# Kernel tuning notes

Hardware: AMD Instinct MI355X
Metric: run time of the kernel (lower is better)

The kernel has to match this reference:

```python
import jax, jax.numpy as jnp
import numpy as np

MARGIN = 0.5
BETA = 0.0
K = 5

def setup_inputs() -> dict:
    key = jax.random.key(0)
    k1, k2 = jax.random.split(key)
    n, d, n_classes = 4096, 512, 512
    inputs = jax.random.normal(k1, (n, d), dtype=jnp.float32)
    # L2-normalize as is standard for similarity-based DML embeddings
    inputs = inputs / jnp.linalg.norm(inputs, axis=1, keepdims=True)
    targets = jax.random.randint(k2, (n,), 0, n_classes, dtype=jnp.int64)
    return {"inputs": inputs, "targets": targets}

def reference(inputs, targets):
    n = inputs.shape[0]
    sim = inputs @ inputs.T                      # [n, n] similarity matrix
    same = targets[:, None] == targets[None, :]  # [n, n] same-class mask
    eye = jnp.eye(n, dtype=bool)
    pos_mask = same & ~eye                       # positive pairs (off-diagonal)
    neg_mask = ~same                             # negative pairs
    # margin_loss (hinge on similarity): pos -> [margin + beta - s]_+, neg -> [margin + s - beta]_+
    pos_l = jnp.maximum(MARGIN + BETA - sim, 0.0)
    neg_l = jnp.maximum(MARGIN + sim - BETA, 0.0)
    valid = pos_mask | neg_mask
    pair_loss = jnp.where(pos_mask, pos_l, neg_l)  # per-pair loss where valid
    num_of_zeros = jnp.sum(valid & (pair_loss == 0.0))
    # top-(4K) over the multiset of all valid pair losses (== topk of concat(pos_loss, neg_loss))
    masked = jnp.where(valid, pair_loss, -jnp.inf).reshape(-1)
    top_loss, _ = jax.lax.top_k(masked, 4 * K)
    loss = jnp.mean(top_loss)
    mean_pos_sim = jnp.sum(jnp.where(pos_mask, sim, 0.0)) / jnp.sum(pos_mask)
    mean_neg_sim = jnp.sum(jnp.where(neg_mask, sim, 0.0)) / jnp.sum(neg_mask)
    # NOTE: the original swaps the names: it returns mean(pos_sim) as `mean_neg_sim` and vice versa.
    return (loss, num_of_zeros, mean_pos_sim, mean_neg_sim)
```

## Files before the change

kernel.cpp:

```cpp
#include <hip/hip_runtime.h>
#include <hip/hip_fp16.h>

constexpr int N = 4096;
constexpr int D = 512;
constexpr int NT = 32;
constexpr int NBLK = NT * (NT + 1) / 2;
constexpr float SENT = -1e30f;
constexpr unsigned TCV = 8386560u;

constexpr float T0 = 0.60f;
constexpr unsigned CCAP = 320;

typedef _Float16 f16x8 __attribute__((ext_vector_type(8)));
typedef float f32x4 __attribute__((ext_vector_type(4)));

__device__ __forceinline__ void load_lds16(const _Float16* g, _Float16* l) {
  __builtin_amdgcn_global_load_lds(
      (const __attribute__((address_space(1))) void*)g,
      (__attribute__((address_space(3))) void*)l, 16, 0, 0);
}

template <int M>
__device__ __forceinline__ void wave_sel10(float (&vals)[M], float (&out)[10]) {
  int lane = threadIdx.x & 63;
  float lm = vals[0];
#pragma unroll
  for (int k = 1; k < M; k++) lm = fmaxf(lm, vals[k]);
#pragma unroll
  for (int r = 0; r < 10; r++) {
    float wmx = lm;
#pragma unroll
    for (int ofs = 1; ofs < 64; ofs <<= 1)
      wmx = fmaxf(wmx, __shfl_xor(wmx, ofs));
    out[r] = wmx;
    unsigned long long b = __ballot(lm == wmx);
    int leader = __ffsll(b) - 1;
    if (lane == leader) {
      bool found = false;
#pragma unroll
      for (int k = 0; k < M; k++) {
        bool hit = !found && (vals[k] == wmx);
        vals[k] = hit ? SENT : vals[k];
        found = found || hit;
      }
      lm = vals[0];
#pragma unroll
      for (int k = 1; k < M; k++) lm = fmaxf(lm, vals[k]);
    }
  }
}

constexpr int TOP10G_IDX = 1584;
constexpr int XH_OFF = 32768;

__global__ void prep_kernel(const float4* __restrict__ X4,
                            ushort4* __restrict__ Xh4) {
  int gid = blockIdx.x * 256 + threadIdx.x;
  float4 v = X4[gid];
  ushort4 o;
  o.x = __half_as_ushort(__float2half_rn(v.x));
  o.y = __half_as_ushort(__float2half_rn(v.y));
  o.z = __half_as_ushort(__float2half_rn(v.z));
  o.w = __half_as_ushort(__float2half_rn(v.w));
  Xh4[gid] = o;
}

__global__ __launch_bounds__(256, 3) void gemm_stats_kernel(
    const _Float16* __restrict__ Xh, const int* __restrict__ tgt,
    float* __restrict__ slots, float* __restrict__ top10g) {
  __shared__ _Float16 As[2][128 * 32];
  __shared__ _Float16 Bs[2][128 * 32];
  __shared__ int tA[128], tB[128];
  __shared__ float redf[2][4];
  __shared__ unsigned redu[4];
  __shared__ float wml[40];
  __shared__ float cbuf[CCAP];
  __shared__ unsigned ccnt;

  int tid = threadIdx.x;
  if (tid == 0) ccnt = 0u;

  int id = blockIdx.x, br = 0;
  while (id >= (NT - br)) { id -= (NT - br); br++; }
  int bc = br + id;

  if (tid < 128) tA[tid] = tgt[br * 128 + tid];
  else tB[tid - 128] = tgt[bc * 128 + (tid - 128)];

  int lane = tid & 63, wave = tid >> 6;
  int wm2 = (wave >> 1) << 6;
  int wn2 = (wave & 1) << 6;
  int lrow = lane & 15;
  int q4 = lane >> 4;
  int xk = (lrow >> 1) & 3;
  int quad4 = q4 * 4;

  int srow[2], scol[2], sdst[2];
#pragma unroll
  for (int i = 0; i < 2; i++) {
    int C = i * 256 + tid;
    int row = C >> 2, p = C & 3;
    srow[i] = row;
    scol[i] = (p ^ ((row >> 1) & 3)) * 8;
    sdst[i] = (i * 4 + wave) * 512;
  }
  const _Float16* Arow = Xh + (size_t)(br * 128) * D;
  const _Float16* Brow = Xh + (size_t)(bc * 128) * D;

#pragma unroll
  for (int i = 0; i < 2; i++) {
    load_lds16(Arow + srow[i] * D + scol[i], &As[0][sdst[i]]);
    load_lds16(Brow + srow[i] * D + scol[i], &Bs[0][sdst[i]]);
  }

  f32x4 acc[4][4] = {};
#pragma unroll
  for (int t = 0; t < 16; t++) {
    int cur = t & 1;
    __syncthreads();
    if (t < 15) {
      int k0 = (t + 1) * 32;
#pragma unroll
      for (int i = 0; i < 2; i++) {
        load_lds16(Arow + srow[i] * D + k0 + scol[i], &As[cur ^ 1][sdst[i]]);
        load_lds16(Brow + srow[i] * D + k0 + scol[i], &Bs[cur ^ 1][sdst[i]]);
      }
    }
    f16x8 af[4], bf[4];
#pragma unroll
    for (int mi = 0; mi < 4; mi++)
      af[mi] = *(const f16x8*)&As[cur][(wm2 + mi * 16 + lrow) * 32 +
                                       (q4 ^ xk) * 8];
#pragma unroll
    for (int ni = 0; ni < 4; ni++)
      bf[ni] = *(const f16x8*)&Bs[cur][(wn2 + ni * 16 + lrow) * 32 +
                                       (q4 ^ xk) * 8];
#pragma unroll
    for (int mi = 0; mi < 4; mi++)
#pragma unroll
      for (int ni = 0; ni < 4; ni++)
        acc[mi][ni] = __builtin_amdgcn_mfma_f32_16x16x32_f16(
            af[mi], bf[ni], acc[mi][ni], 0, 0, 0);
  }

  int tj[4];
#pragma unroll
  for (int ni = 0; ni < 4; ni++) tj[ni] = tB[wn2 + ni * 16 + lrow];

  float lsv = 0.f, lsp = 0.f;
  unsigned cz = 0;
  int ib = br * 128 + wm2 + quad4;
  int jb = bc * 128 + wn2 + lrow;
#pragma unroll
  for (int mi = 0; mi < 4; mi++) {
#pragma unroll
    for (int r = 0; r < 4; r++) {
      int trow = tA[wm2 + mi * 16 + quad4 + r];
      int i = ib + mi * 16 + r;
#pragma unroll
      for (int ni = 0; ni < 4; ni++) {
        float s = acc[mi][ni][r];
        int j = jb + ni * 16;
        bool valid = j > i;
        bool pos = valid && (trow == tj[ni]);
        float loss = fmaxf(0.5f + (pos ? -s : s), 0.0f);
        if (valid) {
          lsv += s;
          if (loss == 0.0f) cz += 0x10000u;
          if (loss >= T0) {
            unsigned p = atomicAdd(&ccnt, 1u);
            if (p < CCAP) cbuf[p] = loss;
          }
        }
        if (pos) { lsp += s; cz += 1u; }
      }
    }
  }
#pragma unroll
  for (int o = 32; o > 0; o >>= 1) {
    lsv += __shfl_down(lsv, o);
    lsp += __shfl_down(lsp, o);
    cz += __shfl_down(cz, o);
  }
  if (lane == 0) {
    redf[0][wave] = lsv; redf[1][wave] = lsp; redu[wave] = cz;
  }
  __syncthreads();

  if (tid == 192) {
    float a = 0.f, b = 0.f;
    unsigned c = 0;
#pragma unroll
    for (int w = 0; w < 4; w++) { a += redf[0][w]; b += redf[1][w]; c += redu[w]; }
    slots[blockIdx.x] = a;
    slots[NBLK + blockIdx.x] = b;
    ((unsigned*)slots)[2 * NBLK + blockIdx.x] = c;
  }

  unsigned cc = ccnt;
  if (cc >= 10u && cc <= CCAP) {
    if (wave == 0) {
      float m5[5];
#pragma unroll
      for (int k = 0; k < 5; k++) {
        unsigned g = lane + k * 64u;
        m5[k] = (g < cc) ? cbuf[g] : SENT;
      }
      float b10[10];
      wave_sel10<5>(m5, b10);
      if (lane == 0) {
#pragma unroll
        for (int r = 0; r < 10; r++) top10g[blockIdx.x * 10 + r] = b10[r];
      }
    }
  } else {
    float vals[64];
#pragma unroll
    for (int mi = 0; mi < 4; mi++) {
#pragma unroll
      for (int r = 0; r < 4; r++) {
        int trow = tA[wm2 + mi * 16 + quad4 + r];
        int i = ib + mi * 16 + r;
#pragma unroll
        for (int ni = 0; ni < 4; ni++) {
          float s = acc[mi][ni][r];
          int j = jb + ni * 16;
          bool valid = j > i;
          bool pos = valid && (trow == tj[ni]);
          float loss = fmaxf(0.5f + (pos ? -s : s), 0.0f);
          vals[(mi * 4 + ni) * 4 + r] = valid ? loss : SENT;
        }
      }
    }
    float wl[10];
    wave_sel10<64>(vals, wl);
    if (lane == 0) {
#pragma unroll
      for (int r = 0; r < 10; r++) wml[wave * 10 + r] = wl[r];
    }
    __syncthreads();
    if (wave == 0) {
      float m1[1];
      m1[0] = (lane < 40) ? wml[lane] : SENT;
      float b10[10];
      wave_sel10<1>(m1, b10);
      if (lane == 0) {
#pragma unroll
        for (int r = 0; r < 10; r++) top10g[blockIdx.x * 10 + r] = b10[r];
      }
    }
  }
}

__global__ __launch_bounds__(1024) void finalize_kernel(
    const float* __restrict__ slots, const float* __restrict__ top10g,
    float* __restrict__ out) {
  __shared__ float wml[160];
  __shared__ float redf[2][16];
  __shared__ unsigned redu[2][16];

  int tid = threadIdx.x, lane = tid & 63, wave = tid >> 6;

  float sv = 0.f, sp = 0.f;
  unsigned cv = 0, zz = 0;
  if (tid < NBLK) {
    sv = slots[tid];
    sp = slots[NBLK + tid];
    unsigned c = ((const unsigned*)slots)[2 * NBLK + tid];
    cv = c & 0xffffu;
    zz = c >> 16;
  }

  float v6[6];
#pragma unroll
  for (int k = 0; k < 6; k++) {
    int g = tid + k * 1024;
    v6[k] = (g < NBLK * 10) ? top10g[g] : SENT;
  }

#pragma unroll
  for (int o = 32; o > 0; o >>= 1) {
    sv += __shfl_down(sv, o);
    sp += __shfl_down(sp, o);
    cv += __shfl_down(cv, o);
    zz += __shfl_down(zz, o);
  }
  if (lane == 0) {
    redf[0][wave] = sv; redf[1][wave] = sp;
    redu[0][wave] = cv; redu[1][wave] = zz;
  }

  float wl[10];
  wave_sel10<6>(v6, wl);
  if (lane == 0) {
#pragma unroll
    for (int r = 0; r < 10; r++) wml[wave * 10 + r] = wl[r];
  }
  __syncthreads();

  if (wave == 0) {
    float m3[3];
#pragma unroll
    for (int k = 0; k < 3; k++) {
      int g = lane + k * 64;
      m3[k] = (g < 160) ? wml[g] : SENT;
    }
    float f10[10];
    wave_sel10<3>(m3, f10);
    if (lane == 0) {
      float topsum = 0.f;
#pragma unroll
      for (int r = 0; r < 10; r++) topsum += f10[r];
      float tsv = 0.f, tsp = 0.f;
      unsigned tcv = 0, tzz = 0;
#pragma unroll
      for (int w = 0; w < 16; w++) {
        tsv += redf[0][w]; tsp += redf[1][w];
        tcv += redu[0][w]; tzz += redu[1][w];
      }
      out[0] = topsum * 0.1f;
      out[1] = (float)(2u * tzz);
      out[2] = tsp / (float)tcv;
      out[3] = (tsv - tsp) / (float)(TCV - tcv);
    }
  }
}

extern "C" void kernel_launch(void* const* d_in, const int* in_sizes, int n_in,
                              void* d_out, int out_size, void* d_ws,
                              size_t ws_size, hipStream_t stream) {
  const float* X = (const float*)d_in[0];
  const int* tgt = (const int*)d_in[1];
  float* out = (float*)d_out;
  char* ws = (char*)d_ws;

  float* slots = (float*)ws;
  float* top10g = slots + TOP10G_IDX;
  _Float16* Xh = (_Float16*)(ws + XH_OFF);

  prep_kernel<<<(N * D / 4) / 256, 256, 0, stream>>>((const float4*)X,
                                                     (ushort4*)Xh);
  gemm_stats_kernel<<<NBLK, 256, 0, stream>>>(Xh, tgt, slots, top10g);
  finalize_kernel<<<1, 1024, 0, stream>>>(slots, top10g, out);
}
```

Measured before the change: 97.54 us.

## Triple-buffer GEMM loads, batch candidate atomics, binary-search fallback, prune finalize top-k

```diff
diff --git a/kernel.cpp b/kernel.cpp
--- a/kernel.cpp
+++ b/kernel.cpp
@@ -50,7 +50,8 @@
   }
 }
 
-constexpr int TOP10G_IDX = 1584;
+constexpr int BMAX_IDX = 3 * NBLK;
+constexpr int TOP10G_IDX = 4 * NBLK;
 constexpr int XH_OFF = 32768;
 
 __global__ void prep_kernel(const float4* __restrict__ X4,
@@ -68,14 +69,16 @@
 __global__ __launch_bounds__(256, 3) void gemm_stats_kernel(
     const _Float16* __restrict__ Xh, const int* __restrict__ tgt,
     float* __restrict__ slots, float* __restrict__ top10g) {
-  __shared__ _Float16 As[2][128 * 32];
-  __shared__ _Float16 Bs[2][128 * 32];
+  __shared__ _Float16 As[3][128 * 32];
+  __shared__ _Float16 Bs[3][128 * 32];
   __shared__ int tA[128], tB[128];
   __shared__ float redf[2][4];
   __shared__ unsigned redu[4];
-  __shared__ float wml[40];
+  __shared__ float redm[4];
+  __shared__ unsigned redc[4];
   __shared__ float cbuf[CCAP];
   __shared__ unsigned ccnt;
+  __shared__ unsigned scc;
 
   int tid = threadIdx.x;
   if (tid == 0) ccnt = 0u;
@@ -112,29 +115,40 @@
     load_lds16(Arow + srow[i] * D + scol[i], &As[0][sdst[i]]);
     load_lds16(Brow + srow[i] * D + scol[i], &Bs[0][sdst[i]]);
   }
+#pragma unroll
+  for (int i = 0; i < 2; i++) {
+    load_lds16(Arow + srow[i] * D + 32 + scol[i], &As[1][sdst[i]]);
+    load_lds16(Brow + srow[i] * D + 32 + scol[i], &Bs[1][sdst[i]]);
+  }
 
   f32x4 acc[4][4] = {};
 #pragma unroll
   for (int t = 0; t < 16; t++) {
-    int cur = t & 1;
-    __syncthreads();
     if (t < 15) {
-      int k0 = (t + 1) * 32;
+      asm volatile("s_waitcnt vmcnt(4) lgkmcnt(0)" ::: "memory");
+    } else {
+      asm volatile("s_waitcnt vmcnt(0) lgkmcnt(0)" ::: "memory");
+    }
+    __builtin_amdgcn_s_barrier();
+    if (t < 14) {
+      int k0 = (t + 2) * 32;
+      int nb = (t + 2) % 3;
 #pragma unroll
       for (int i = 0; i < 2; i++) {
-        load_lds16(Arow + srow[i] * D + k0 + scol[i], &As[cur ^ 1][sdst[i]]);
-        load_lds16(Brow + srow[i] * D + k0 + scol[i], &Bs[cur ^ 1][sdst[i]]);
-      }
-    }
+        load_lds16(Arow + srow[i] * D + k0 + scol[i], &As[nb][sdst[i]]);
+        load_lds16(Brow + srow[i] * D + k0 + scol[i], &Bs[nb][sdst[i]]);
+      }
+    }
+    int b = t % 3;
     f16x8 af[4], bf[4];
 #pragma unroll
     for (int mi = 0; mi < 4; mi++)
-      af[mi] = *(const f16x8*)&As[cur][(wm2 + mi * 16 + lrow) * 32 +
-                                       (q4 ^ xk) * 8];
+      af[mi] = *(const f16x8*)&As[b][(wm2 + mi * 16 + lrow) * 32 +
+                                     (q4 ^ xk) * 8];
 #pragma unroll
     for (int ni = 0; ni < 4; ni++)
-      bf[ni] = *(const f16x8*)&Bs[cur][(wn2 + ni * 16 + lrow) * 32 +
-                                       (q4 ^ xk) * 8];
+      bf[ni] = *(const f16x8*)&Bs[b][(wn2 + ni * 16 + lrow) * 32 +
+                                     (q4 ^ xk) * 8];
 #pragma unroll
     for (int mi = 0; mi < 4; mi++)
 #pragma unroll
@@ -146,75 +160,10 @@
   int tj[4];
 #pragma unroll
   for (int ni = 0; ni < 4; ni++) tj[ni] = tB[wn2 + ni * 16 + lrow];
-
-  float lsv = 0.f, lsp = 0.f;
-  unsigned cz = 0;
   int ib = br * 128 + wm2 + quad4;
   int jb = bc * 128 + wn2 + lrow;
-#pragma unroll
-  for (int mi = 0; mi < 4; mi++) {
-#pragma unroll
-    for (int r = 0; r < 4; r++) {
-      int trow = tA[wm2 + mi * 16 + quad4 + r];
-      int i = ib + mi * 16 + r;
-#pragma unroll
-      for (int ni = 0; ni < 4; ni++) {
-        float s = acc[mi][ni][r];
-        int j = jb + ni * 16;
-        bool valid = j > i;
-        bool pos = valid && (trow == tj[ni]);
-        float loss = fmaxf(0.5f + (pos ? -s : s), 0.0f);
-        if (valid) {
-          lsv += s;
-          if (loss == 0.0f) cz += 0x10000u;
-          if (loss >= T0) {
-            unsigned p = atomicAdd(&ccnt, 1u);
-            if (p < CCAP) cbuf[p] = loss;
-          }
-        }
-        if (pos) { lsp += s; cz += 1u; }
-      }
-    }
-  }
-#pragma unroll
-  for (int o = 32; o > 0; o >>= 1) {
-    lsv += __shfl_down(lsv, o);
-    lsp += __shfl_down(lsp, o);
-    cz += __shfl_down(cz, o);
-  }
-  if (lane == 0) {
-    redf[0][wave] = lsv; redf[1][wave] = lsp; redu[wave] = cz;
-  }
-  __syncthreads();
-
-  if (tid == 192) {
-    float a = 0.f, b = 0.f;
-    unsigned c = 0;
-#pragma unroll
-    for (int w = 0; w < 4; w++) { a += redf[0][w]; b += redf[1][w]; c += redu[w]; }
-    slots[blockIdx.x] = a;
-    slots[NBLK + blockIdx.x] = b;
-    ((unsigned*)slots)[2 * NBLK + blockIdx.x] = c;
-  }
-
-  unsigned cc = ccnt;
-  if (cc >= 10u && cc <= CCAP) {
-    if (wave == 0) {
-      float m5[5];
-#pragma unroll
-      for (int k = 0; k < 5; k++) {
-        unsigned g = lane + k * 64u;
-        m5[k] = (g < cc) ? cbuf[g] : SENT;
-      }
-      float b10[10];
-      wave_sel10<5>(m5, b10);
-      if (lane == 0) {
-#pragma unroll
-        for (int r = 0; r < 10; r++) top10g[blockIdx.x * 10 + r] = b10[r];
-      }
-    }
-  } else {
-    float vals[64];
+
+  auto forEachLoss = [&](auto&& fn) {
 #pragma unroll
     for (int mi = 0; mi < 4; mi++) {
 #pragma unroll
@@ -228,26 +177,124 @@
           bool valid = j > i;
           bool pos = valid && (trow == tj[ni]);
           float loss = fmaxf(0.5f + (pos ? -s : s), 0.0f);
-          vals[(mi * 4 + ni) * 4 + r] = valid ? loss : SENT;
+          fn(s, loss, valid, pos);
         }
       }
     }
-    float wl[10];
-    wave_sel10<64>(vals, wl);
+  };
+
+  float lsv = 0.f, lsp = 0.f, tmax = SENT;
+  unsigned cz = 0, cc = 0;
+  float b0 = 0.f, b1 = 0.f, b2 = 0.f, b3 = 0.f;
+  forEachLoss([&](float s, float loss, bool valid, bool pos) {
+    if (valid) {
+      lsv += s;
+      if (loss == 0.0f) cz += 0x10000u;
+      tmax = fmaxf(tmax, loss);
+      if (loss >= T0) {
+        if (cc == 0) b0 = loss;
+        else if (cc == 1) b1 = loss;
+        else if (cc == 2) b2 = loss;
+        else if (cc == 3) b3 = loss;
+        else {
+          unsigned op = atomicAdd(&ccnt, 1u);
+          if (op < CCAP) cbuf[op] = loss;
+        }
+        cc++;
+      }
+    }
+    if (pos) { lsp += s; cz += 1u; }
+  });
+
+  float lmax = tmax;
+#pragma unroll
+  for (int o = 32; o > 0; o >>= 1) {
+    lsv += __shfl_down(lsv, o);
+    lsp += __shfl_down(lsp, o);
+    cz += __shfl_down(cz, o);
+    lmax = fmaxf(lmax, __shfl_down(lmax, o));
+  }
+  if (lane == 0) {
+    redf[0][wave] = lsv; redf[1][wave] = lsp;
+    redu[wave] = cz; redm[wave] = lmax;
+  }
+
+  unsigned cnt4 = cc < 4u ? cc : 4u;
+  unsigned inc = cnt4;
+#pragma unroll
+  for (int o = 1; o < 64; o <<= 1) {
+    unsigned tt = __shfl_up(inc, o);
+    if (lane >= o) inc += tt;
+  }
+  unsigned base = 0;
+  if (lane == 63) base = atomicAdd(&ccnt, inc);
+  base = __shfl(base, 63);
+  unsigned p = base + inc - cnt4;
+  if (cnt4 > 0u && p < CCAP) cbuf[p] = b0;
+  if (cnt4 > 1u && p + 1 < CCAP) cbuf[p + 1] = b1;
+  if (cnt4 > 2u && p + 2 < CCAP) cbuf[p + 2] = b2;
+  if (cnt4 > 3u && p + 3 < CCAP) cbuf[p + 3] = b3;
+  __syncthreads();
+
+  if (tid == 192) {
+    float a = redf[0][0] + redf[0][1] + redf[0][2] + redf[0][3];
+    float b = redf[1][0] + redf[1][1] + redf[1][2] + redf[1][3];
+    unsigned c = redu[0] + redu[1] + redu[2] + redu[3];
+    float bm = fmaxf(fmaxf(redm[0], redm[1]), fmaxf(redm[2], redm[3]));
+    slots[blockIdx.x] = a;
+    slots[NBLK + blockIdx.x] = b;
+    ((unsigned*)slots)[2 * NBLK + blockIdx.x] = c;
+    slots[BMAX_IDX + blockIdx.x] = bm;
+  }
+
+  unsigned cct = ccnt;
+  if (cct < 10u || cct > CCAP) {
+    unsigned lo = 0u, hi = 0x7f800000u;
+    while (hi - lo > 1u) {
+      unsigned mid = lo + (hi - lo) / 2u;
+      float Tm = __uint_as_float(mid);
+      unsigned c = 0;
+      forEachLoss([&](float s, float loss, bool valid, bool pos) {
+        (void)s; (void)pos;
+        if (valid && loss >= Tm) c++;
+      });
+#pragma unroll
+      for (int o = 32; o > 0; o >>= 1) c += __shfl_down(c, o);
+      if (lane == 0) redc[wave] = c;
+      __syncthreads();
+      if (tid == 0) scc = redc[0] + redc[1] + redc[2] + redc[3];
+      __syncthreads();
+      if (scc >= 10u) lo = mid; else hi = mid;
+    }
+    float Tq = __uint_as_float(lo);
+    if (tid == 0) ccnt = 0u;
+    __syncthreads();
+    forEachLoss([&](float s, float loss, bool valid, bool pos) {
+      (void)s; (void)pos;
+      if (valid && loss > Tq) {
+        unsigned op = atomicAdd(&ccnt, 1u);
+        if (op < CCAP) cbuf[op] = loss;
+      }
+    });
+    __syncthreads();
+    unsigned m = ccnt;
+    if (tid < 10) cbuf[m + tid] = Tq;
+    __syncthreads();
+    cct = m + 10u;
+  }
+
+  if (wave == 0) {
+    float m5[5];
+#pragma unroll
+    for (int k = 0; k < 5; k++) {
+      unsigned g = lane + k * 64u;
+      m5[k] = (g < cct) ? cbuf[g] : SENT;
+    }
+    float b10[10];
+    wave_sel10<5>(m5, b10);
     if (lane == 0) {
 #pragma unroll
-      for (int r = 0; r < 10; r++) wml[wave * 10 + r] = wl[r];
-    }
-    __syncthreads();
-    if (wave == 0) {
-      float m1[1];
-      m1[0] = (lane < 40) ? wml[lane] : SENT;
-      float b10[10];
-      wave_sel10<1>(m1, b10);
-      if (lane == 0) {
-#pragma unroll
-        for (int r = 0; r < 10; r++) top10g[blockIdx.x * 10 + r] = b10[r];
-      }
+      for (int r = 0; r < 10; r++) top10g[blockIdx.x * 10 + r] = b10[r];
     }
   }
 }
@@ -258,8 +305,13 @@
   __shared__ float wml[160];
   __shared__ float redf[2][16];
   __shared__ unsigned redu[2][16];
+  __shared__ int blist[64];
+  __shared__ unsigned bcnt;
+  __shared__ float gbuf[640];
+  __shared__ float sT;
 
   int tid = threadIdx.x, lane = tid & 63, wave = tid >> 6;
+  if (tid == 0) bcnt = 0u;
 
   float sv = 0.f, sp = 0.f;
   unsigned cv = 0, zz = 0;
@@ -270,14 +322,7 @@
     cv = c & 0xffffu;
     zz = c >> 16;
   }
-
-  float v6[6];
-#pragma unroll
-  for (int k = 0; k < 6; k++) {
-    int g = tid + k * 1024;
-    v6[k] = (g < NBLK * 10) ? top10g[g] : SENT;
-  }
-
+  float bm = (tid < NBLK) ? slots[BMAX_IDX + tid] : SENT;
 #pragma unroll
   for (int o = 32; o > 0; o >>= 1) {
     sv += __shfl_down(sv, o);
@@ -290,14 +335,15 @@
     redu[0][wave] = cv; redu[1][wave] = zz;
   }
 
+  float v1[1];
+  v1[0] = bm;
   float wl[10];
-  wave_sel10<6>(v6, wl);
+  wave_sel10<1>(v1, wl);
   if (lane == 0) {
 #pragma unroll
     for (int r = 0; r < 10; r++) wml[wave * 10 + r] = wl[r];
   }
   __syncthreads();
-
   if (wave == 0) {
     float m3[3];
 #pragma unroll
@@ -305,24 +351,75 @@
       int g = lane + k * 64;
       m3[k] = (g < 160) ? wml[g] : SENT;
     }
-    float f10[10];
-    wave_sel10<3>(m3, f10);
+    float t10[10];
+    wave_sel10<3>(m3, t10);
+    if (lane == 0) sT = t10[9];
+  }
+  __syncthreads();
+  float T = sT;
+
+  if (tid < NBLK && bm >= T) {
+    unsigned p = atomicAdd(&bcnt, 1u);
+    if (p < 64u) blist[p] = tid;
+  }
+  __syncthreads();
+  unsigned nb = bcnt;
+
+  float f10[10];
+  if (nb <= 64u) {
+    unsigned ng = nb * 10u;
+    if ((unsigned)tid < ng)
+      gbuf[tid] = top10g[(unsigned)blist[tid / 10u] * 10u + tid % 10u];
+    __syncthreads();
+    if (wave == 0) {
+      float mA[10];
+#pragma unroll
+      for (int k = 0; k < 10; k++) {
+        unsigned g = lane + k * 64u;
+        mA[k] = (g < ng) ? gbuf[g] : SENT;
+      }
+      wave_sel10<10>(mA, f10);
+    }
+  } else {
+    float v6[6];
+#pragma unroll
+    for (int k = 0; k < 6; k++) {
+      int g = tid + k * 1024;
+      v6[k] = (g < NBLK * 10) ? top10g[g] : SENT;
+    }
+    float wl2[10];
+    wave_sel10<6>(v6, wl2);
     if (lane == 0) {
-      float topsum = 0.f;
-#pragma unroll
-      for (int r = 0; r < 10; r++) topsum += f10[r];
-      float tsv = 0.f, tsp = 0.f;
-      unsigned tcv = 0, tzz = 0;
-#pragma unroll
-      for (int w = 0; w < 16; w++) {
-        tsv += redf[0][w]; tsp += redf[1][w];
-        tcv += redu[0][w]; tzz += redu[1][w];
-      }
-      out[0] = topsum * 0.1f;
-      out[1] = (float)(2u * tzz);
-      out[2] = tsp / (float)tcv;
-      out[3] = (tsv - tsp) / (float)(TCV - tcv);
-    }
+#pragma unroll
+      for (int r = 0; r < 10; r++) wml[wave * 10 + r] = wl2[r];
+    }
+    __syncthreads();
+    if (wave == 0) {
+      float m3[3];
+#pragma unroll
+      for (int k = 0; k < 3; k++) {
+        int g = lane + k * 64;
+        m3[k] = (g < 160) ? wml[g] : SENT;
+      }
+      wave_sel10<3>(m3, f10);
+    }
+  }
+
+  if (wave == 0 && lane == 0) {
+    float topsum = 0.f;
+#pragma unroll
+    for (int r = 0; r < 10; r++) topsum += f10[r];
+    float tsv = 0.f, tsp = 0.f;
+    unsigned tcv = 0, tzz = 0;
+#pragma unroll
+    for (int w = 0; w < 16; w++) {
+      tsv += redf[0][w]; tsp += redf[1][w];
+      tcv += redu[0][w]; tzz += redu[1][w];
+    }
+    out[0] = topsum * 0.1f;
+    out[1] = (float)(2u * tzz);
+    out[2] = tsp / (float)tcv;
+    out[3] = (tsv - tsp) / (float)(TCV - tcv);
   }
 }
 
```

After: 108.0 us. 1.11x slower.
